# Optimization experiments

Hardware: AMD Instinct MI355X
Metric: run time of the kernel (lower is better)

The kernel has to match this reference:

```python
import jax, jax.numpy as jnp
import numpy as np
from jax import lax

H = W = 1024            # input frame size
STRIDE = 16             # backbone total stride (4 stride-2 convs)
FH = FW = H // STRIDE   # 64x64 feature map
A = 3                   # anchors per cell
SIZES = (32.0, 64.0, 128.0)
K = 100                 # fixed NMS candidate count (jit-static)
SCORE_TH = 0.5          # kwargs['threshhold']
IOU_TH = 0.5
BORDER = 4              # draw_boxes border_size=4


def _conv(x, w, b, stride):
    y = lax.conv_general_dilated(x, w, (stride, stride), 'SAME',
                                 dimension_numbers=('NCHW', 'OIHW', 'NCHW'))
    return y + b[None, :, None, None]


def _anchors():
    ys, xs = jnp.meshgrid(jnp.arange(FH, dtype=jnp.float32),
                          jnp.arange(FW, dtype=jnp.float32), indexing='ij')
    cx = (xs + 0.5) * STRIDE
    cy = (ys + 0.5) * STRIDE
    sz = jnp.asarray(SIZES, dtype=jnp.float32)
    cx = jnp.broadcast_to(cx[:, :, None], (FH, FW, A))
    cy = jnp.broadcast_to(cy[:, :, None], (FH, FW, A))
    ww = jnp.broadcast_to(sz[None, None, :], (FH, FW, A))
    return jnp.stack([cx, cy, ww, ww], -1).reshape(-1, 4)  # [N,4] cx,cy,w,h


def _facenet(frame, w1, b1, w2, b2, w3, b3, w4, b4, wh, bh):
    x = jax.nn.relu(_conv(frame, w1, b1, 2))   # [1,32,512,512]
    x = jax.nn.relu(_conv(x, w2, b2, 2))       # [1,64,256,256]
    x = jax.nn.relu(_conv(x, w3, b3, 2))       # [1,128,128,128]
    x = jax.nn.relu(_conv(x, w4, b4, 2))       # [1,256,64,64]
    p = _conv(x, wh, bh, 1)                    # [1,A*5,64,64]
    p = p.reshape(A, 5, FH, FW).transpose(2, 3, 0, 1).reshape(-1, 5)  # [N,5]
    t, logit = p[:, :4], p[:, 4]
    a = _anchors()
    cx = a[:, 0] + t[:, 0] * a[:, 2]
    cy = a[:, 1] + t[:, 1] * a[:, 3]
    bw = a[:, 2] * jnp.exp(jnp.clip(t[:, 2], -4.0, 4.0))
    bhh = a[:, 3] * jnp.exp(jnp.clip(t[:, 3], -4.0, 4.0))
    boxes = jnp.stack([cx - bw * 0.5, cy - bhh * 0.5,
                       cx + bw * 0.5, cy + bhh * 0.5], -1)  # [N,4] xyxy
    scores = jax.nn.sigmoid(logit)             # [N]
    return boxes, scores


def _pairwise_iou(b):
    area = (b[:, 2] - b[:, 0]) * (b[:, 3] - b[:, 1])
    lt = jnp.maximum(b[:, None, :2], b[None, :, :2])
    rb = jnp.minimum(b[:, None, 2:], b[None, :, 2:])
    wh2 = jnp.clip(rb - lt, 0.0)
    inter = wh2[..., 0] * wh2[..., 1]
    return inter / (area[:, None] + area[None, :] - inter + 1e-9)


def _nms(boxes, scores):
    s = jnp.where(scores >= SCORE_TH, scores, -1.0)
    top, idx = lax.top_k(s, K)
    b = boxes[idx]                    # [K,4], score-sorted
    valid = top > 0.0
    ious = _pairwise_iou(b)           # [K,K]
    rng = jnp.arange(K)

    def body(i, keep):
        sup = (ious[i] > IOU_TH) & keep[i] & (rng > i)
        return keep & (~sup)

    keep = lax.fori_loop(0, K, body, valid)
    return b, keep


def _draw(frame, boxes, keep):
    x1 = jnp.clip(boxes[:, 0], 0.0, W)[:, None, None]
    y1 = jnp.clip(boxes[:, 1], 0.0, H)[:, None, None]
    x2 = jnp.clip(boxes[:, 2], 0.0, W)[:, None, None]
    y2 = jnp.clip(boxes[:, 3], 0.0, H)[:, None, None]
    ys = jnp.arange(H, dtype=jnp.float32)[None, :, None]
    xs = jnp.arange(W, dtype=jnp.float32)[None, None, :]
    inside = (ys >= y1) & (ys < y2) & (xs >= x1) & (xs < x2)
    inner = (ys >= y1 + BORDER) & (ys < y2 - BORDER) & \
            (xs >= x1 + BORDER) & (xs < x2 - BORDER)
    border = inside & (~inner) & keep[:, None, None]   # [K,H,W]
    mask = jnp.any(border, axis=0)                     # [H,W]
    red = jnp.array([1.0, 0.0, 0.0], dtype=frame.dtype)[None, :, None, None]
    return jnp.where(mask[None, None, :, :], red, frame)


def setup_inputs() -> dict:
    key = jax.random.key(0)
    ks = jax.random.split(key, 12)
    sc = 0.05
    return {
        'frame': jax.random.normal(ks[0], (1, 3, H, W), jnp.float32),
        'w1': jax.random.normal(ks[1], (32, 3, 3, 3), jnp.float32) * sc,
        'b1': jax.random.normal(ks[2], (32,), jnp.float32) * sc,
        'w2': jax.random.normal(ks[3], (64, 32, 3, 3), jnp.float32) * sc,
        'b2': jax.random.normal(ks[4], (64,), jnp.float32) * sc,
        'w3': jax.random.normal(ks[5], (128, 64, 3, 3), jnp.float32) * sc,
        'b3': jax.random.normal(ks[6], (128,), jnp.float32) * sc,
        'w4': jax.random.normal(ks[7], (256, 128, 3, 3), jnp.float32) * sc,
        'b4': jax.random.normal(ks[8], (256,), jnp.float32) * sc,
        'wh': jax.random.normal(ks[9], (A * 5, 256, 3, 3), jnp.float32) * sc,
        'bh': jax.random.normal(ks[10], (A * 5,), jnp.float32) * sc,
    }


def reference(frame, w1, b1, w2, b2, w3, b3, w4, b4, wh, bh):
    boxes, scores = _facenet(frame, w1, b1, w2, b2, w3, b3, w4, b4, wh, bh)
    kept_boxes, keep = _nms(boxes, scores)     # kwargs: use_nms=True, only_anchors=False
    im = _draw(frame, kept_boxes, keep)        # border_size=4, color='red'
    return im
```

## Files before the change

kernel.cpp:

```cpp
#include <hip/hip_runtime.h>


constexpr int KTOP  = 100;
constexpr int NANCH = 12288;

template<int CIN, int HIN, int WIN, int STRIDE, int COB, int CICHUNK, bool FUSEOUT>
__global__ __launch_bounds__(256)
void convk(const float* __restrict__ in, const float* __restrict__ w,
           const float* __restrict__ bias, float* __restrict__ out, int CO)
{
    constexpr int HOUT = (STRIDE == 2) ? HIN / 2 : HIN;
    constexpr int WOUT = (STRIDE == 2) ? WIN / 2 : WIN;
    constexpr int NPX  = HOUT * WOUT;
    constexpr int SPR  = WOUT / 64;

    const int lane = threadIdx.x & 63;
    const int seg  = blockIdx.x * 4 + (threadIdx.x >> 6);
    const int oy   = seg / SPR;
    const int ox   = (seg - oy * SPR) * 64 + lane;
    const int co0  = blockIdx.y * COB;
    const int ci0  = blockIdx.z * CICHUNK;

    float acc[COB];
#pragma unroll
    for (int c = 0; c < COB; ++c) acc[c] = 0.f;

    size_t ro[3];
    bool   rm[3];
#pragma unroll
    for (int ky = 0; ky < 3; ++ky) {
        const int iy = (STRIDE == 2) ? (2 * oy + ky) : (oy + ky - 1);
        rm[ky] = (iy >= 0) && (iy < HIN);
        const int iyc = iy < 0 ? 0 : (iy > HIN - 1 ? HIN - 1 : iy);
        ro[ky] = (size_t)iyc * WIN;
    }
    int  xa, xb, xc;
    bool ma, mc;
    if constexpr (STRIDE == 2) {
        xa = 2 * ox;
        xb = 0;
        mc = (2 * ox + 2) < WIN;
        xc = mc ? 2 * ox + 2 : WIN - 1;
        ma = true;
    } else {
        ma = ox > 0;
        xa = ma ? ox - 1 : 0;
        xb = ox;
        mc = ox < WIN - 1;
        xc = mc ? ox + 1 : WIN - 1;
    }

    for (int cii = 0; cii < CICHUNK; ++cii) {
        const int ci = ci0 + cii;
        const float* __restrict__ cp = in + (size_t)ci * (HIN * WIN);
#pragma unroll
        for (int ky = 0; ky < 3; ++ky) {
            float t0, t1, t2;
            if constexpr (STRIDE == 2) {
                const float2 p = *reinterpret_cast<const float2*>(cp + ro[ky] + xa);
                const float  e = cp[ro[ky] + xc];
                t0 = rm[ky] ? p.x : 0.f;
                t1 = rm[ky] ? p.y : 0.f;
                t2 = (rm[ky] && mc) ? e : 0.f;
            } else {
                const float a = cp[ro[ky] + xa];
                const float b = cp[ro[ky] + xb];
                const float e = cp[ro[ky] + xc];
                t0 = (rm[ky] && ma) ? a : 0.f;
                t1 = rm[ky] ? b : 0.f;
                t2 = (rm[ky] && mc) ? e : 0.f;
            }
#pragma unroll
            for (int co = 0; co < COB; ++co) {
                const float* __restrict__ wp =
                    w + (((size_t)(co0 + co) * CIN + ci) * 3 + ky) * 3;
                acc[co] = fmaf(t0, wp[0], acc[co]);
                acc[co] = fmaf(t1, wp[1], acc[co]);
                acc[co] = fmaf(t2, wp[2], acc[co]);
            }
        }
    }

    const int op = oy * WOUT + ox;
#pragma unroll
    for (int co = 0; co < COB; ++co) {
        if constexpr (FUSEOUT) {
            out[(size_t)(co0 + co) * NPX + op] =
                fmaxf(acc[co] + bias[co0 + co], 0.f);
        } else {
            out[((size_t)blockIdx.z * CO + co0 + co) * NPX + op] = acc[co];
        }
    }
}

template<int NCHUNK, int NPX, bool RELU>
__global__ __launch_bounds__(256)
void reducek(const float* __restrict__ part, const float* __restrict__ bias,
             float* __restrict__ out, int CO)
{
    const int t = blockIdx.x * 256 + threadIdx.x;
    const int co = t / NPX, px = t - co * NPX;
    float s = 0.f;
#pragma unroll
    for (int c = 0; c < NCHUNK; ++c) s += part[((size_t)c * CO + co) * NPX + px];
    s += bias[co];
    out[(size_t)co * NPX + px] = RELU ? fmaxf(s, 0.f) : s;
}

__global__ void decode_kernel(const float* __restrict__ head,
                              float4* __restrict__ boxes,
                              unsigned long long* __restrict__ keys)
{
    const int i = blockIdx.x * 256 + threadIdx.x;
    const int a = i % 3;
    const int xy = i / 3;
    const int x = xy & 63, y = xy >> 6;
    const int px = y * 64 + x;

    const float t0 = head[(a * 5 + 0) * 4096 + px];
    const float t1 = head[(a * 5 + 1) * 4096 + px];
    const float t2 = head[(a * 5 + 2) * 4096 + px];
    const float t3 = head[(a * 5 + 3) * 4096 + px];
    const float lg = head[(a * 5 + 4) * 4096 + px];

    const float sz  = (a == 0) ? 32.f : (a == 1) ? 64.f : 128.f;
    const float cxa = (x + 0.5f) * 16.f;
    const float cya = (y + 0.5f) * 16.f;

    const float cx = __fadd_rn(cxa, __fmul_rn(t0, sz));
    const float cy = __fadd_rn(cya, __fmul_rn(t1, sz));
    const float bw = __fmul_rn(sz, expf(fminf(fmaxf(t2, -4.f), 4.f)));
    const float bh = __fmul_rn(sz, expf(fminf(fmaxf(t3, -4.f), 4.f)));
    const float hw = __fmul_rn(bw, 0.5f);
    const float hh = __fmul_rn(bh, 0.5f);

    float4 bb;
    bb.x = __fsub_rn(cx, hw);
    bb.y = __fsub_rn(cy, hh);
    bb.z = __fadd_rn(cx, hw);
    bb.w = __fadd_rn(cy, hh);
    boxes[i] = bb;

    const float score = 1.f / (1.f + expf(-lg));
    unsigned long long key = 0ull;
    if (score >= 0.5f) {
        key = ((unsigned long long)__float_as_uint(score) << 32)
            | (unsigned long long)(0xFFFFFFFFu - (unsigned)i);
    }
    keys[i] = key;
}

constexpr int JSPLIT = 16;
constexpr int JCHUNK = NANCH / JSPLIT;

__global__ __launch_bounds__(256)
void rank_kernel(const unsigned long long* __restrict__ keys,
                 int* __restrict__ rank)
{
    const int i = blockIdx.x * 256 + threadIdx.x;
    const unsigned long long ki = keys[i];
    const int lane = threadIdx.x & 63;
    const int jbase = blockIdx.y * JCHUNK;

    int cnt = 0;
    for (int g = 0; g < JCHUNK / 64; ++g) {
        const unsigned long long kj = keys[jbase + g * 64 + lane];
        const unsigned lo0 = (unsigned)kj;
        const unsigned hi0 = (unsigned)(kj >> 32);
#pragma unroll
        for (int l = 0; l < 64; ++l) {
            const unsigned lo = (unsigned)__builtin_amdgcn_readlane((int)lo0, l);
            const unsigned hi = (unsigned)__builtin_amdgcn_readlane((int)hi0, l);
            const unsigned long long kjj = ((unsigned long long)hi << 32) | lo;
            cnt += (kjj > ki) ? 1 : 0;
        }
    }
    if (cnt) atomicAdd(&rank[i], cnt);
}

__global__ void scatter_kernel(const unsigned long long* __restrict__ keys,
                               const int* __restrict__ rank,
                               const float4* __restrict__ boxes,
                               float4* __restrict__ selb, int* __restrict__ selv)
{
    const int i = blockIdx.x * 256 + threadIdx.x;
    if (keys[i] == 0ull) return;
    const int r = rank[i];
    if (r < KTOP) { selb[r] = boxes[i]; selv[r] = 1; }
}

__global__ __launch_bounds__(128)
void nms_kernel(const float4* __restrict__ selb, const int* __restrict__ selv,
                float4* __restrict__ drawb)
{
    __shared__ float bx1[KTOP], by1[KTOP], bx2[KTOP], by2[KTOP], ar[KTOP];
    __shared__ int kp[KTOP];
    const int t = threadIdx.x;
    if (t < KTOP) {
        const float4 b = selb[t];
        bx1[t] = b.x; by1[t] = b.y; bx2[t] = b.z; by2[t] = b.w;
        ar[t] = (b.z - b.x) * (b.w - b.y);
        kp[t] = selv[t];
    }
    __syncthreads();
    for (int i = 0; i < KTOP - 1; ++i) {
        if (t > i && t < KTOP) {
            if (kp[i] && kp[t]) {
                const float lx = fmaxf(bx1[i], bx1[t]);
                const float ly = fmaxf(by1[i], by1[t]);
                const float rx = fminf(bx2[i], bx2[t]);
                const float ry = fminf(by2[i], by2[t]);
                const float ww = fmaxf(rx - lx, 0.f);
                const float hh = fmaxf(ry - ly, 0.f);
                const float inter = ww * hh;
                const float iou = inter / (ar[i] + ar[t] - inter + 1e-9f);
                if (iou > 0.5f) kp[t] = 0;
            }
        }
        __syncthreads();
    }
    if (t < KTOP) {
        float4 d;
        if (kp[t]) {
            d.x = fminf(fmaxf(bx1[t], 0.f), 1024.f);
            d.y = fminf(fmaxf(by1[t], 0.f), 1024.f);
            d.z = fminf(fmaxf(bx2[t], 0.f), 1024.f);
            d.w = fminf(fmaxf(by2[t], 0.f), 1024.f);
        } else {
            d.x = 3e9f; d.y = 3e9f; d.z = -3e9f; d.w = -3e9f;
        }
        drawb[t] = d;
    }
}

__global__ __launch_bounds__(256)
void draw_kernel(const float* __restrict__ frame,
                 const float4* __restrict__ drawb, float* __restrict__ out)
{
    const int y = blockIdx.x >> 2;
    const int x = ((blockIdx.x & 3) << 8) + threadIdx.x;
    const float fy = (float)y, fx = (float)x;

    bool mask = false;
#pragma unroll 1
    for (int b = 0; b < KTOP; ++b) {
        const float4 d = drawb[b];
        if (fy >= d.y && fy < d.w) {
            const bool yinner = (fy >= d.y + 4.f) && (fy < d.w - 4.f);
            const bool xin    = (fx >= d.x) && (fx < d.z);
            const bool xinner = (fx >= d.x + 4.f) && (fx < d.z - 4.f);
            mask |= xin && !(yinner && xinner);
        }
    }
    const int p = y * 1024 + x;
    const float f0 = frame[p];
    const float f1 = frame[1048576 + p];
    const float f2 = frame[2097152 + p];
    out[p]           = mask ? 1.f : f0;
    out[1048576 + p] = mask ? 0.f : f1;
    out[2097152 + p] = mask ? 0.f : f2;
}

extern "C" void kernel_launch(void* const* d_in, const int* in_sizes, int n_in,
                              void* d_out, int out_size, void* d_ws, size_t ws_size,
                              hipStream_t stream)
{
    const float* frame = (const float*)d_in[0];
    const float* w1 = (const float*)d_in[1];  const float* b1 = (const float*)d_in[2];
    const float* w2 = (const float*)d_in[3];  const float* b2 = (const float*)d_in[4];
    const float* w3 = (const float*)d_in[5];  const float* b3 = (const float*)d_in[6];
    const float* w4 = (const float*)d_in[7];  const float* b4 = (const float*)d_in[8];
    const float* wh = (const float*)d_in[9];  const float* bh = (const float*)d_in[10];

    char* ws = (char*)d_ws;
    float* buf1  = (float*)ws;
    float* buf2  = (float*)(ws + 33554432);
    float* part3 = (float*)ws;
    float* buf3  = (float*)(ws + 16777216);
    float* part4 = (float*)ws;
    float* buf4  = (float*)(ws + 25165824);
    float* partH = (float*)ws;
    float* heado = (float*)(ws + 8388608);
    char*  D     = ws + 33554432;
    float4* boxes = (float4*)(D);
    unsigned long long* keys = (unsigned long long*)(D + 196608);
    int*    rankb = (int*)(D + 294912);
    int*    selv  = (int*)(D + 344064);
    float4* selb  = (float4*)(D + 344576);
    float4* drawb = (float4*)(D + 346176);
    float*  outp  = (float*)d_out;

    convk<3,  1024, 1024, 2, 8, 3,  true ><<<dim3(1024, 4, 1), 256, 0, stream>>>(frame, w1, b1, buf1, 32);
    convk<32,  512,  512, 2, 8, 32, true ><<<dim3(256,  8, 1), 256, 0, stream>>>(buf1, w2, b2, buf2, 64);

    convk<64,  256,  256, 2, 8, 32, false><<<dim3(64, 16, 2), 256, 0, stream>>>(buf2, w3, nullptr, part3, 128);
    reducek<2, 16384, true><<<8192, 256, 0, stream>>>(part3, b3, buf3, 128);

    convk<128, 128,  128, 2, 8, 32, false><<<dim3(16, 32, 4), 256, 0, stream>>>(buf3, w4, nullptr, part4, 256);
    reducek<4, 4096, true><<<4096, 256, 0, stream>>>(part4, b4, buf4, 256);

    convk<256, 64, 64, 1, 15, 8, false><<<dim3(16, 1, 32), 256, 0, stream>>>(buf4, wh, nullptr, partH, 15);
    reducek<32, 4096, false><<<240, 256, 0, stream>>>(partH, bh, heado, 15);

    hipMemsetAsync(rankb, 0, 49152 + 512, stream);

    decode_kernel<<<48, 256, 0, stream>>>(heado, boxes, keys);
    rank_kernel<<<dim3(48, JSPLIT), 256, 0, stream>>>(keys, rankb);
    scatter_kernel<<<48, 256, 0, stream>>>(keys, rankb, boxes, selb, selv);
    nms_kernel<<<1, 128, 0, stream>>>(selb, selv, drawb);
    draw_kernel<<<4096, 256, 0, stream>>>(frame, drawb, outp);
}
```

Baseline: 403.7 us.

## Stage conv weights in LDS and software-pipeline input loads across channels

Each block now copies its slice of conv weights into shared memory once, then reads weights from LDS instead of global memory inside the FMA loop. The channel loop is also software-pipelined: the next channel's 9 input taps are loaded while the current channel's FMAs run. Together these aim to reduce global weight-load traffic and hide input-load latency, at the cost of extra registers, LDS use and a block-wide barrier.

After: 404.3 us. No clear change (+0.2%).

```diff
diff --git a/kernel.cpp b/kernel.cpp
--- a/kernel.cpp
+++ b/kernel.cpp
@@ -13,6 +13,9 @@
     constexpr int WOUT = (STRIDE == 2) ? WIN / 2 : WIN;
     constexpr int NPX  = HOUT * WOUT;
     constexpr int SPR  = WOUT / 64;
+    constexpr int NW   = COB * CICHUNK * 9;
+
+    __shared__ float lw[NW];
 
     const int lane = threadIdx.x & 63;
     const int seg  = blockIdx.x * 4 + (threadIdx.x >> 6);
@@ -21,9 +24,14 @@
     const int co0  = blockIdx.y * COB;
     const int ci0  = blockIdx.z * CICHUNK;
 
-    float acc[COB];
-#pragma unroll
-    for (int c = 0; c < COB; ++c) acc[c] = 0.f;
+    for (int idx = threadIdx.x; idx < NW; idx += 256) {
+        const int cii = idx / (COB * 9);
+        const int r   = idx - cii * (COB * 9);
+        const int co  = r / 9;
+        const int k   = r - co * 9;
+        lw[idx] = w[((size_t)(co0 + co) * CIN + (ci0 + cii)) * 9 + k];
+    }
+    __syncthreads();
 
     size_t ro[3];
     bool   rm[3];
@@ -38,10 +46,9 @@
     bool ma, mc;
     if constexpr (STRIDE == 2) {
         xa = 2 * ox;
-        xb = 0;
+        xb = 0; ma = true;
         mc = (2 * ox + 2) < WIN;
         xc = mc ? 2 * ox + 2 : WIN - 1;
-        ma = true;
     } else {
         ma = ox > 0;
         xa = ma ? ox - 1 : 0;
@@ -50,35 +57,61 @@
         xc = mc ? ox + 1 : WIN - 1;
     }
 
-    for (int cii = 0; cii < CICHUNK; ++cii) {
-        const int ci = ci0 + cii;
-        const float* __restrict__ cp = in + (size_t)ci * (HIN * WIN);
+    auto loadraw = [&](int ci, float* r) {
+        const float* __restrict__ cp = in + (size_t)ci * ((size_t)HIN * WIN);
 #pragma unroll
         for (int ky = 0; ky < 3; ++ky) {
-            float t0, t1, t2;
             if constexpr (STRIDE == 2) {
                 const float2 p = *reinterpret_cast<const float2*>(cp + ro[ky] + xa);
-                const float  e = cp[ro[ky] + xc];
-                t0 = rm[ky] ? p.x : 0.f;
-                t1 = rm[ky] ? p.y : 0.f;
-                t2 = (rm[ky] && mc) ? e : 0.f;
+                r[3 * ky + 0] = p.x;
+                r[3 * ky + 1] = p.y;
+                r[3 * ky + 2] = cp[ro[ky] + xc];
             } else {
-                const float a = cp[ro[ky] + xa];
-                const float b = cp[ro[ky] + xb];
-                const float e = cp[ro[ky] + xc];
-                t0 = (rm[ky] && ma) ? a : 0.f;
-                t1 = rm[ky] ? b : 0.f;
-                t2 = (rm[ky] && mc) ? e : 0.f;
+                r[3 * ky + 0] = cp[ro[ky] + xa];
+                r[3 * ky + 1] = cp[ro[ky] + xb];
+                r[3 * ky + 2] = cp[ro[ky] + xc];
             }
-#pragma unroll
-            for (int co = 0; co < COB; ++co) {
-                const float* __restrict__ wp =
-                    w + (((size_t)(co0 + co) * CIN + ci) * 3 + ky) * 3;
-                acc[co] = fmaf(t0, wp[0], acc[co]);
-                acc[co] = fmaf(t1, wp[1], acc[co]);
-                acc[co] = fmaf(t2, wp[2], acc[co]);
-            }
-        }
+        }
+    };
+    auto sel = [&](const float* r, float* t) {
+#pragma unroll
+        for (int ky = 0; ky < 3; ++ky) {
+            t[3 * ky + 0] = (rm[ky] && ma) ? r[3 * ky + 0] : 0.f;
+            t[3 * ky + 1] = rm[ky] ? r[3 * ky + 1] : 0.f;
+            t[3 * ky + 2] = (rm[ky] && mc) ? r[3 * ky + 2] : 0.f;
+        }
+    };
+
+    float acc[COB];
+#pragma unroll
+    for (int c = 0; c < COB; ++c) acc[c] = 0.f;
+
+    auto fmas = [&](int cii, const float* t) {
+        const float* __restrict__ lwp = &lw[cii * COB * 9];
+#pragma unroll
+        for (int co = 0; co < COB; ++co) {
+#pragma unroll
+            for (int k = 0; k < 9; ++k)
+                acc[co] = fmaf(t[k], lwp[co * 9 + k], acc[co]);
+        }
+    };
+
+    float rc[9];
+    loadraw(ci0, rc);
+#pragma unroll 2
+    for (int cii = 0; cii < CICHUNK - 1; ++cii) {
+        float tc[9];
+        sel(rc, tc);
+        float rn[9];
+        loadraw(ci0 + cii + 1, rn);
+        fmas(cii, tc);
+#pragma unroll
+        for (int k = 0; k < 9; ++k) rc[k] = rn[k];
+    }
+    {
+        float tc[9];
+        sel(rc, tc);
+        fmas(CICHUNK - 1, tc);
     }
 
     const int op = oy * WOUT + ox;
```
